# Kernel tuning notes

Measured on AMD Instinct MI355X. Metric: run time of the kernel, lower is better.

The kernel has to match this reference:

```python
import jax, jax.numpy as jnp
import numpy as np

V, D, L, H, FF, B, S = 32000, 2048, 4, 16, 8192, 2, 2048
DH = D // H
PRUNE_LAYERS = (1, 2)   # layers with an attached pruning module
KEEP_RATIO = 0.5        # keep_ratio arg of forward_prefill_with_pruning


def _rms(x, w, eps=1e-6):
    return x * w * jax.lax.rsqrt(jnp.mean(x * x, -1, keepdims=True) + eps)


def _rope(x):
    # x: [B,H,s,DH]; position_ids = arange(s), recomputed after every pruning step
    s = x.shape[2]
    half = DH // 2
    inv = 1.0 / (10000.0 ** (jnp.arange(half, dtype=jnp.float32) / half))
    ang = jnp.arange(s, dtype=jnp.float32)[:, None] * inv  # [s, half]
    cos, sin = jnp.cos(ang), jnp.sin(ang)
    x1, x2 = x[..., :half], x[..., half:]
    return jnp.concatenate([x1 * cos - x2 * sin, x1 * sin + x2 * cos], -1)


def _block(h, mask, wq, wk, wv, wo, wg, wu, wd, ln1, ln2):
    b, s, _ = h.shape
    hn = _rms(h, ln1)
    q = _rope((hn @ wq).reshape(b, s, H, DH).transpose(0, 2, 1, 3))
    k = _rope((hn @ wk).reshape(b, s, H, DH).transpose(0, 2, 1, 3))
    v = (hn @ wv).reshape(b, s, H, DH).transpose(0, 2, 1, 3)
    att = jnp.einsum('bhqd,bhkd->bhqk', q, k) / np.float32(np.sqrt(DH))
    allowed = jnp.tril(jnp.ones((s, s), bool)) & (mask[:, None, None, :] > 0)
    att = jnp.where(allowed, att, jnp.float32(-1e9))
    o = jnp.einsum('bhqk,bhkd->bhqd', jax.nn.softmax(att, -1), v)
    h = h + o.transpose(0, 2, 1, 3).reshape(b, s, D) @ wo
    hn = _rms(h, ln2)
    h = h + (jax.nn.silu(hn @ wg) * (hn @ wu)) @ wd
    return h


def _forward(input_ids, attention_mask, embed, wq, wk, wv, wo, wg, wu, wd, ln1, ln2, lnf, lm_head, scorer):
    h = embed[input_ids]        # [B,S,D]
    mask = attention_mask
    for i in range(L):
        if i in PRUNE_LAYERS:
            pi = PRUNE_LAYERS.index(i)
            # pruning module: Linear(D->2); keep score = logits[..., 0]
            sc = jnp.einsum('bsd,cd->bsc', h, scorer[pi])[..., 0]
            kk = max(1, int(h.shape[1] * KEEP_RATIO))      # static under jit
            _, idx = jax.lax.top_k(sc, kk)
            idx = jnp.sort(idx, -1)                        # sorted kept indices
            h = jnp.take_along_axis(h, idx[..., None], axis=1)
            mask = jnp.take_along_axis(mask, idx, axis=1)
        h = _block(h, mask, wq[i], wk[i], wv[i], wo[i], wg[i], wu[i], wd[i], ln1[i], ln2[i])
    return _rms(h, lnf) @ lm_head   # logits [B, S_pruned, V]


def setup_inputs() -> dict:
    key = jax.random.key(0)
    ks = jax.random.split(key, 12)
    g = lambda k, shape: jax.random.normal(k, shape, jnp.float32) * 0.02
    return {
        'input_ids': jax.random.randint(ks[0], (B, S), 0, V, jnp.int32),
        'attention_mask': jnp.ones((B, S), jnp.int32),
        'embed': g(ks[1], (V, D)),
        'wq': g(ks[2], (L, D, D)),
        'wk': g(ks[3], (L, D, D)),
        'wv': g(ks[4], (L, D, D)),
        'wo': g(ks[5], (L, D, D)),
        'wg': g(ks[6], (L, D, FF)),
        'wu': g(ks[7], (L, D, FF)),
        'wd': g(ks[8], (L, FF, D)),
        'ln1': jnp.ones((L, D), jnp.float32),
        'ln2': jnp.ones((L, D), jnp.float32),
        'lnf': jnp.ones((D,), jnp.float32),
        'lm_head': g(ks[9], (D, V)),
        'scorer': g(ks[10], (len(PRUNE_LAYERS), 2, D)),
    }


def reference(input_ids, attention_mask, embed, wq, wk, wv, wo, wg, wu, wd, ln1, ln2, lnf, lm_head, scorer):
    return _forward(input_ids, attention_mask, embed, wq, wk, wv, wo, wg, wu, wd, ln1, ln2, lnf, lm_head, scorer)
```

## Files before the change

kernel.cpp:

```cpp
#include <hip/hip_runtime.h>
#include <math.h>


#define DD 2048
#define HH 16
#define DHH 128
#define FFF 8192
#define BBATCH 2
#define SSEQ 2048
#define VV 32000
#define LLAYERS 4

typedef float4 f4;
typedef __attribute__((ext_vector_type(8))) short short8;
typedef __attribute__((ext_vector_type(4))) float f32x4;
typedef unsigned short u16;

__device__ inline u16 bf16rne(float x) {
    unsigned u = __float_as_uint(x);
    unsigned r = (u + 0x7FFFu + ((u >> 16) & 1u)) >> 16;
    return (u16)r;
}
__device__ inline float bf16tof(u16 h) {
    return __uint_as_float(((unsigned)h) << 16);
// ... 73 lines not shown
        u16* hp = (u16*)&hv; u16* lp = (u16*)&lv;
#pragma unroll
        for (int j = 0; j < 4; j++) {
            u16 h = bf16rne(o[j]);
            hp[j] = h;
            lp[j] = bf16rne(o[j] - bf16tof(h));
        }
        *(ushort4*)&OH[(size_t)row * DD + i * 4] = hv;
        *(ushort4*)&OL[(size_t)row * DD + i * 4] = lv;
    }
}

__global__ __launch_bounds__(256) void k_cvt_w(const float* __restrict__ W,
                                               u16* __restrict__ WtH,
                                               u16* __restrict__ WtL,
                                               int K, int N, int nc0, int dn0,
                                               int writeLo) {
    __shared__ float T[64][65];
    int tid = threadIdx.x;
    int n0g = nc0 + blockIdx.x * 64;
    int k0  = blockIdx.y * 64;
#pragma unroll
    for (int it = 0; it < 4; it++) {
        int r = it * 16 + (tid >> 4);
        int c4 = (tid & 15) * 4;
        f4 v = *(const f4*)(W + (size_t)(k0 + r) * N + n0g + c4);
        T[r][c4 + 0] = v.x; T[r][c4 + 1] = v.y;
        T[r][c4 + 2] = v.z; T[r][c4 + 3] = v.w;
    }
    __syncthreads();
    int nl = tid >> 2;
    int ks = (tid & 3) * 16;
    u16 hi[16], lo[16];
#pragma unroll
    for (int j = 0; j < 16; j++) {
        float v = T[ks + j][nl];
        u16 h = bf16rne(v);
        hi[j] = h;
        lo[j] = bf16rne(v - bf16tof(h));
    }
    size_t base = (size_t)(dn0 + blockIdx.x * 64 + nl) * K + k0 + ks;
    *(short8*)&WtH[base]     = *(short8*)&hi[0];
    *(short8*)&WtH[base + 8] = *(short8*)&hi[8];
    if (writeLo) {
        *(short8*)&WtL[base]     = *(short8*)&lo[0];
        *(short8*)&WtL[base + 8] = *(short8*)&lo[8];
    }
}

template <int PASSES, int RES, int DUAL>
__global__ __launch_bounds__(256, 2) void k_bgemm(const u16* __restrict__ AH,
                                                  const u16* __restrict__ AL,
                                                  const u16* __restrict__ B1H,
                                                  const u16* __restrict__ B1L,
                                                  const u16* __restrict__ B2H,
                                                  const u16* __restrict__ B2L,
                                                  const float* __restrict__ Rsrc,
                                                  float* __restrict__ C,
                                                  u16* __restrict__ OH,
                                                  u16* __restrict__ OL,
                                                  int M, int ldC, int K) {
    constexpr int NW = DUAL ? 2 : 1;
    __shared__ u16 As[128 * 32];
    __shared__ u16 Bs[NW][128 * 32];
    int tid = threadIdx.x;
    int bx = blockIdx.x, by = blockIdx.y;
    xcd_swz(bx, by);
    int m0 = by * 128, n0 = bx * 128;
    int lane = tid & 63, w = tid >> 6;
    int wm = w >> 1, wn = w & 1;
    int lr = lane & 15, lq = lane >> 4;
    int grow = lane >> 2;
    int gcol = (lane & 3) * 8;

    f32x4 acc[NW][4][4];
#pragma unroll
    for (int u = 0; u < NW; u++)
#pragma unroll
        for (int i = 0; i < 4; i++)
#pragma unroll
            for (int j = 0; j < 4; j++)
#pragma unroll
                for (int r = 0; r < 4; r++) acc[u][i][j][r] = 0.f;

    const int KT = PASSES * K;
    for (int kb = 0; kb < KT; kb += 32) {
        int p  = (PASSES > 1) ? ((kb >= 2 * K) ? 2 : ((kb >= K) ? 1 : 0)) : 0;
        int ks = kb - p * K;
        const u16* Ab = ((p == 2) ? AL  : AH)  + (size_t)(m0 + w * 32) * K + ks;
        const u16* Bb = ((p == 1) ? B1L : B1H) + (size_t)(n0 + w * 32) * K + ks;
        __syncthreads();
        gload16(Ab + (size_t)grow * K + gcol,        &As[w * 1024]);
        gload16(Ab + (size_t)(grow + 16) * K + gcol, &As[w * 1024 + 512]);
        gload16(Bb + (size_t)grow * K + gcol,        &Bs[0][w * 1024]);
        gload16(Bb + (size_t)(grow + 16) * K + gcol, &Bs[0][w * 1024 + 512]);
        if constexpr (DUAL) {
            const u16* B2b = ((p == 1) ? B2L : B2H) + (size_t)(n0 + w * 32) * K + ks;
            gload16(B2b + (size_t)grow * K + gcol,        &Bs[1][w * 1024]);
            gload16(B2b + (size_t)(grow + 16) * K + gcol, &Bs[1][w * 1024 + 512]);
        }
        __syncthreads();
        short8 a[4];
#pragma unroll
        for (int i = 0; i < 4; i++)
            a[i] = *(const short8*)&As[(wm * 64 + i * 16 + lr) * 32 + lq * 8];
#pragma unroll
        for (int u = 0; u < NW; u++) {
#pragma unroll
            for (int j = 0; j < 4; j++) {
                short8 b = *(const short8*)&Bs[u][(wn * 64 + j * 16 + lr) * 32 + lq * 8];
#pragma unroll
                for (int i = 0; i < 4; i++)
                    acc[u][i][j] = __builtin_amdgcn_mfma_f32_16x16x32_bf16(
                        a[i], b, acc[u][i][j], 0, 0, 0);
            }
        }
    }
#pragma unroll
    for (int i = 0; i < 4; i++) {
#pragma unroll
        for (int j = 0; j < 4; j++) {
            int gm = m0 + wm * 64 + i * 16 + lq * 4;
            int gn = n0 + wn * 64 + j * 16 + lr;
#pragma unroll
            for (int r = 0; r < 4; r++) {
                size_t off = (size_t)(gm + r) * ldC + gn;
                if constexpr (DUAL) {
                    float g = acc[0][i][j][r], uu = acc[1][i][j][r];
                    float v = g / (1.0f + expf(-g)) * uu;
                    u16 h = bf16rne(v);
                    OH[off] = h;
                    OL[off] = bf16rne(v - bf16tof(h));
                } else {
                    float v = acc[0][i][j][r];
                    if constexpr (RES) v += Rsrc[off];
                    C[off] = v;
                }
            }
        }
    }
}

template <int PASSES, int PLANE, int EPI>
__global__ __launch_bounds__(512, 2) void k_bg256(const u16* __restrict__ AH,
                                                  const u16* __restrict__ AL,
                                                  const u16* __restrict__ BH,
                                                  const u16* __restrict__ BL,
                                                  float* __restrict__ C,
                                                  u16* __restrict__ OH,
                                                  u16* __restrict__ OL,
                                                  const u16* __restrict__ GEH,
                                                  const u16* __restrict__ GEL,
                                                  int M, int ldC, int K, int ld) {
    __shared__ u16 SM[65536];
    int tid = threadIdx.x;
    int bx = blockIdx.x, by = blockIdx.y;
    xcd_swz(bx, by);
    {
        size_t zo = (size_t)blockIdx.z * K;
        AH += zo; BH += zo;
        if constexpr (PASSES > 1) { AL += zo; BL += zo; }
        if constexpr (!PLANE) C += (size_t)blockIdx.z * ((size_t)M * ldC);
    }
    int m0 = by * 256, n0 = bx * 256;
    int w = tid >> 6, lane = tid & 63;
    int wm = w >> 2, wn = w & 3;
    int lr = lane & 15, lq = lane >> 4;

    f32x4 acc[8][4];
#pragma unroll
    for (int i = 0; i < 8; i++)
#pragma unroll
        for (int j = 0; j < 4; j++)
#pragma unroll
            for (int r = 0; r < 4; r++) acc[i][j][r] = 0.f;

    auto ASRC = [&](int T) -> const u16* {
        int kb = T * 64;
        if (PASSES > 1) {
            if (kb >= 2 * K) return AL + (kb - 2 * K);
            if (kb >= K)     return AH + (kb - K);
        }
        return AH + kb;
    };
    auto BSRC = [&](int T) -> const u16* {
        int kb = T * 64;
        if (PASSES > 1) {
            if (kb >= 2 * K) return BH + (kb - 2 * K);
            if (kb >= K)     return BL + (kb - K);
        }
        return BH + kb;
    };
    int srr = lane >> 3;
    int scc = ((lane & 7) ^ srr) * 8;
    auto STAGE_A = [&](int T, int h, int buf) {
        const u16* s = ASRC(T) + (size_t)(m0 + h * 128 + w * 16 + srr) * ld + scc;
        u16* d = SM + buf * 32768 + h * 8192 + w * 16 * 64;
        gload16(s, d);
        gload16(s + (size_t)8 * ld, d + 8 * 64);
    };
    auto STAGE_B = [&](int T, int h, int buf) {
        const u16* s = BSRC(T) + (size_t)(n0 + h * 128 + w * 16 + srr) * ld + scc;
        u16* d = SM + buf * 32768 + 16384 + h * 8192 + w * 16 * 64;
        gload16(s, d);
        gload16(s + (size_t)8 * ld, d + 8 * 64);
    };
    auto RD_A = [&](const u16* SMb, int MH, short8 (&aF)[4][2]) {
        const u16* Ab = SMb + MH * 8192;
#pragma unroll
        for (int i = 0; i < 4; i++)
#pragma unroll
            for (int kk = 0; kk < 2; kk++)
                aF[i][kk] = *(const short8*)&Ab[(wm * 64 + i * 16 + lr) * 64 +
                                                (((kk * 4 + lq) ^ (lr & 7)) * 8)];
    };
    auto RD_B = [&](const u16* SMb, int NH, short8 (&bF)[2][2]) {
        const u16* Bb = SMb + 16384 + NH * 8192;
#pragma unroll
        for (int j = 0; j < 2; j++)
#pragma unroll
            for (int kk = 0; kk < 2; kk++)
                bF[j][kk] = *(const short8*)&Bb[(wn * 32 + j * 16 + lr) * 64 +
                                                (((kk * 4 + lq) ^ (lr & 7)) * 8)];
    };

    const int NT = (PASSES * K) >> 6;
    STAGE_A(0, 0, 0); STAGE_B(0, 0, 0);
    STAGE_A(0, 1, 0); STAGE_B(0, 1, 0);
    asm volatile("s_waitcnt vmcnt(0)" ::: "memory");
    BARRIER();

    for (int T = 0; T < NT; T++) {
        int cur = T & 1;
        const u16* SMb = SM + cur * 32768;
        short8 a0[4][2], a1[4][2], b0[2][2], b1[2][2];
        if (T + 1 < NT) { STAGE_A(T + 1, 0, cur ^ 1); STAGE_B(T + 1, 0, cur ^ 1); }
        RD_A(SMb, 0, a0);
        RD_B(SMb, 0, b0);
        if (T + 1 < NT) { STAGE_A(T + 1, 1, cur ^ 1); STAGE_B(T + 1, 1, cur ^ 1); }
        RD_B(SMb, 1, b1);
        RD_A(SMb, 1, a1);
        __builtin_amdgcn_s_setprio(1);
#pragma unroll
        for (int kk = 0; kk < 2; kk++)
#pragma unroll
            for (int j = 0; j < 2; j++)
#pragma unroll
                for (int i = 0; i < 4; i++)
                    acc[i][j] = __builtin_amdgcn_mfma_f32_16x16x32_bf16(
                        a0[i][kk], b0[j][kk], acc[i][j], 0, 0, 0);
#pragma unroll
        for (int kk = 0; kk < 2; kk++)
#pragma unroll
            for (int j = 0; j < 2; j++)
#pragma unroll
                for (int i = 0; i < 4; i++)
                    acc[i][2 + j] = __builtin_amdgcn_mfma_f32_16x16x32_bf16(
                        a0[i][kk], b1[j][kk], acc[i][2 + j], 0, 0, 0);
#pragma unroll
        for (int kk = 0; kk < 2; kk++)
#pragma unroll
            for (int j = 0; j < 2; j++)
#pragma unroll
                for (int i = 0; i < 4; i++)
                    acc[4 + i][j] = __builtin_amdgcn_mfma_f32_16x16x32_bf16(
                        a1[i][kk], b0[j][kk], acc[4 + i][j], 0, 0, 0);
#pragma unroll
        for (int kk = 0; kk < 2; kk++)
#pragma unroll
            for (int j = 0; j < 2; j++)
#pragma unroll
                for (int i = 0; i < 4; i++)
                    acc[4 + i][2 + j] = __builtin_amdgcn_mfma_f32_16x16x32_bf16(
                        a1[i][kk], b1[j][kk], acc[4 + i][2 + j], 0, 0, 0);
        __builtin_amdgcn_s_setprio(0);
        if (T + 1 < NT) {
            asm volatile("s_waitcnt vmcnt(0)" ::: "memory");
            BARRIER();
        }
    }

#pragma unroll
    for (int i16 = 0; i16 < 8; i16++) {
#pragma unroll
        for (int jj = 0; jj < 4; jj++) {
            int gm = m0 + (i16 >> 2) * 128 + wm * 64 + (i16 & 3) * 16 + lq * 4;
            int gn = n0 + (jj >> 1) * 128 + wn * 32 + (jj & 1) * 16 + lr;
#pragma unroll
            for (int r = 0; r < 4; r++) {
                size_t off = (size_t)(gm + r) * ldC + gn;
                float v = acc[i16][jj][r];
                if constexpr (PLANE) {
                    if constexpr (EPI) {
                        float g = bf16tof(GEH[off]) + bf16tof(GEL[off]);
                        v = g / (1.0f + expf(-g)) * v;
                    }
                    u16 h = bf16rne(v);
                    OH[off] = h;
                    OL[off] = bf16rne(v - bf16tof(h));
                } else {
                    C[off] = v;
                }
            }
        }
    }
}

__global__ void k_rope_table(float* __restrict__ cosT, float* __restrict__ sinT) {
    int idx = blockIdx.x * blockDim.x + threadIdx.x;
    if (idx >= SSEQ * 64) return;
    int pos = idx >> 6, d = idx & 63;
    float p   = (float)pow(10000.0, (double)d * (1.0 / 64.0));
    float inv = 1.0f / p;
    float ang = (float)pos * inv;
    cosT[idx] = (float)cos((double)ang);
    sinT[idx] = (float)sin((double)ang);
}

__global__ void k_rope(float* __restrict__ C,
                       const float* __restrict__ cosT, const float* __restrict__ sinT,
                       int s, int ld) {
    int bi = blockIdx.x;
    int h = bi % HH;
    int i = (bi / HH) % s;
    size_t base = (size_t)(bi / HH) * ld + h * DHH;
    int d = threadIdx.x;
    float c  = cosT[i * 64 + d];
    float sn = sinT[i * 64 + d];
    float x1 = C[base + d], x2 = C[base + 64 + d];
    C[base + d]      = x1 * c - x2 * sn;
    C[base + 64 + d] = x1 * sn + x2 * c;
    x1 = C[base + 2048 + d]; x2 = C[base + 2048 + 64 + d];
    C[base + 2048 + d]      = x1 * c - x2 * sn;
    C[base + 2048 + 64 + d] = x1 * sn + x2 * c;
}

__global__ __launch_bounds__(256) void k_cvt_qkr(const float* __restrict__ C,
                                                 const float* __restrict__ cosT,
                                                 const float* __restrict__ sinT,
                                                 u16* __restrict__ QHp, u16* __restrict__ QLp,
                                                 u16* __restrict__ KHp, u16* __restrict__ KLp,
                                                 int s) {
    int row = blockIdx.x;
    int i = row % s;
    int c = threadIdx.x * 8;
    int d = c & 127;
    int hi2 = (d >= 64) ? 1 : 0;
    int dd = d - hi2 * 64;
    const float* tb = cosT + (size_t)i * 64;
    const float* ts = sinT + (size_t)i * 64;
#pragma unroll
    for (int sec = 0; sec < 2; sec++) {
        const float* src = C + (size_t)row * 6144 + sec * 2048;
        int base1 = c - hi2 * 64;
        float o[8];
#pragma unroll
        for (int q = 0; q < 2; q++) {
            f4 v1 = *(const f4*)(src + base1 + q * 4);
            f4 v2 = *(const f4*)(src + base1 + 64 + q * 4);
            float a1[4] = {v1.x, v1.y, v1.z, v1.w};
            float a2[4] = {v2.x, v2.y, v2.z, v2.w};
#pragma unroll
            for (int e = 0; e < 4; e++) {
                float cc = tb[dd + q * 4 + e];
                float sn = ts[dd + q * 4 + e];
                o[q * 4 + e] = hi2 ? (a1[e] * sn + a2[e] * cc)
                                   : (a1[e] * cc - a2[e] * sn);
            }
        }
        u16 hbuf[8], lbuf[8];
#pragma unroll
        for (int e = 0; e < 8; e++) {
            u16 h = bf16rne(o[e]);
            hbuf[e] = h;
            lbuf[e] = bf16rne(o[e] - bf16tof(h));
        }
        u16* dh = (sec ? KHp : QHp) + (size_t)row * 2048 + c;
        u16* dl = (sec ? KLp : QLp) + (size_t)row * 2048 + c;
        *(short8*)dh = *(short8*)&hbuf[0];
        *(short8*)dl = *(short8*)&lbuf[0];
    }
}

__global__ __launch_bounds__(256) void k_cvt_vt(const float* __restrict__ C,
                                                u16* __restrict__ VtH,
                                                u16* __restrict__ VtL, int s) {
    __shared__ float T[64][132];
    int bh = blockIdx.y;
    int h = bh & 15, b = bh >> 4;
    int kv0 = blockIdx.x * 64;
    int t = threadIdx.x;
#pragma unroll
    for (int it = 0; it < 8; it++) {
        int kv = it * 8 + (t >> 5);
        int c4 = (t & 31) * 4;
        f4 v = *(const f4*)(C + (size_t)((size_t)b * s + kv0 + kv) * 6144 + 4096 + h * 128 + c4);
        T[kv][c4 + 0] = v.x; T[kv][c4 + 1] = v.y;
        T[kv][c4 + 2] = v.z; T[kv][c4 + 3] = v.w;
    }
    __syncthreads();
    int d = t >> 1, seg = t & 1;
    size_t base = ((size_t)bh * 128 + d) * s + kv0 + seg * 32;
#pragma unroll
    for (int g = 0; g < 4; g++) {
        u16 h8[8], l8[8];
#pragma unroll
        for (int e = 0; e < 8; e++) {
            float v = T[seg * 32 + g * 8 + e][d];
            u16 hh = bf16rne(v);
            h8[e] = hh;
            l8[e] = bf16rne(v - bf16tof(hh));
        }
        int gp = (g ^ ((d >> 1) & 3)) * 8;
        *(short8*)&VtH[base + gp] = *(short8*)&h8[0];
        *(short8*)&VtL[base + gp] = *(short8*)&l8[0];
    }
}

template <int PASSES>
__global__ __launch_bounds__(256, 2) void k_attn_mfma(
        const u16* __restrict__ QHp, const u16* __restrict__ QLp,
        const u16* __restrict__ KHp, const u16* __restrict__ KLp,
        const u16* __restrict__ VtH, const u16* __restrict__ VtL,
        const int* __restrict__ mask,
        u16* __restrict__ OH, u16* __restrict__ OL, int s) {
    constexpr int BUFU = (PASSES > 1) ? 16384 : 8192;
    constexpr int VOFF = (PASSES > 1) ? 8192 : 4096;
    __shared__ u16 SM[2 * BUFU + 5120];
    int tid = threadIdx.x, lane = tid & 63, w = tid >> 6;
    int lr = lane & 15, lq = lane >> 4;
    int grow = lane >> 2;
    int sgcol = (((lane & 3) ^ ((lane >> 3) & 3))) * 8;
    int gcol  = (lane & 3) * 8;
    int rc = (lq ^ ((lr >> 1) & 3)) * 8;
    int gx = gridDim.x;
    int NB = gx * gridDim.y;
    int orig = blockIdx.y * gx + blockIdx.x;
    int qq = NB >> 3, rr = NB & 7;
    int xcd = orig & 7, loc = orig >> 3;
    int swz = (xcd < rr ? xcd * (qq + 1) : rr * (qq + 1) + (xcd - rr) * qq) + loc;
    int bh = swz / gx;
    int qt = gx - 1 - (swz % gx);
    int h = bh & 15, b = bh >> 4;
    int q0 = qt * 128;
// ... 346 lines not shown
                                              int* __restrict__ flg, int s, int kk) {
    int b = blockIdx.x / s, i = blockIdx.x % s;
    const float* scb = sc + (size_t)b * s;
    float vi = scb[i];
    int cnt = 0;
    for (int j = threadIdx.x; j < s; j += 256) {
        float vj = scb[j];
        if (vj > vi || (vj == vi && j < i)) cnt++;
    }
    for (int o = 32; o > 0; o >>= 1) cnt += __shfl_down(cnt, o);
    __shared__ int red[4];
    int wid = threadIdx.x >> 6, lane = threadIdx.x & 63;
    if (lane == 0) red[wid] = cnt;
    __syncthreads();
    if (threadIdx.x == 0) flg[b * s + i] = ((red[0] + red[1] + red[2] + red[3]) < kk) ? 1 : 0;
}

__global__ void k_compact(const int* __restrict__ flg, int* __restrict__ idx, int s, int kk) {
    int b = blockIdx.x;
    if (threadIdx.x == 0) {
        int p = 0;
        for (int i = 0; i < s; i++)
            if (flg[b * s + i]) idx[b * kk + (p++)] = i;
    }
}

__global__ void k_gather(const float* __restrict__ Hin, const int* __restrict__ idx,
                         float* __restrict__ Hout, int s, int kk) {
    int row = blockIdx.x;
    int b = row / kk, p = row % kk;
    int i = idx[b * kk + p];
    const f4* src = (const f4*)(Hin + (size_t)(b * s + i) * DD);
    f4* dst = (f4*)(Hout + (size_t)row * DD);
    for (int t = threadIdx.x; t < DD / 4; t += blockDim.x) dst[t] = src[t];
}

__global__ void k_gather_mask(const int* __restrict__ Min, const int* __restrict__ idx,
                              int* __restrict__ Mout, int s, int kk) {
    int t = blockIdx.x * blockDim.x + threadIdx.x;
    if (t < BBATCH * kk) {
        int b = t / kk, p = t % kk;
        Mout[t] = Min[b * s + idx[b * kk + p]];
    }
}

extern "C" void kernel_launch(void* const* d_in, const int* in_sizes, int n_in,
                              void* d_out, int out_size, void* d_ws, size_t ws_size,
                              hipStream_t stream) {
    const int*   input_ids = (const int*)d_in[0];
    const int*   attn_mask = (const int*)d_in[1];
    const float* embed     = (const float*)d_in[2];
    const float* wq        = (const float*)d_in[3];
    const float* wk        = (const float*)d_in[4];
    const float* wv        = (const float*)d_in[5];
    const float* wo        = (const float*)d_in[6];
    const float* wg        = (const float*)d_in[7];
    const float* wu        = (const float*)d_in[8];
    const float* wd        = (const float*)d_in[9];
    const float* ln1       = (const float*)d_in[10];
    const float* ln2       = (const float*)d_in[11];
    const float* lnf       = (const float*)d_in[12];
    const float* lm_head   = (const float*)d_in[13];
    const float* scorer    = (const float*)d_in[14];

    float* ws = (float*)d_ws;
    const size_t R = (size_t)BBATCH * SSEQ * DD;
    const size_t MISC_FLOATS = 2 * SSEQ * 64 + 5 * (size_t)BBATCH * SSEQ + 1024;
    const size_t NEED_A = (14 * R + MISC_FLOATS) * 4;
    const bool bigws = (ws_size >= NEED_A);

    float* H0   = ws;
    float* H1   = ws + R;
    float* CQKV = ws + 2 * R;
    u16*   AH   = (u16*)(ws + 5 * R);
    u16*   AL   = AH + (size_t)4096 * DD;

    u16* QHp = (u16*)(ws + 6 * R);
    u16* QLp = QHp + (size_t)4096 * DD;
    u16* KHp = (u16*)(ws + 7 * R);
    u16* KLp = KHp + (size_t)4096 * DD;
    u16* VtH = (u16*)(ws + 8 * R);
    u16* VtL = VtH + (size_t)4096 * DD;
    u16* FH  = (u16*)(ws + 6 * R);
    u16* FL  = (u16*)(ws + 8 * R);
    u16* WH1 = (u16*)(ws + 10 * R);
    u16* WL1 = WH1 + (size_t)FFF * DD;
    u16* WH2 = (u16*)(ws + 12 * R);
    u16* WL2 = WH2 + (size_t)FFF * DD;
    u16* WDH = (u16*)(ws + 10 * R);
    u16* WDL = WDH + (size_t)DD * FFF;
    u16* WQKVH = (u16*)(ws + 10 * R);
    u16* WQKVL = WQKVH + (size_t)6144 * DD;

    u16* cWgH = (u16*)CQKV;
    u16* cWgL = cWgH + (size_t)2048 * DD;
    u16* cWuH = cWgL + (size_t)2048 * DD;
    u16* cWuL = cWuH + (size_t)2048 * DD;
    u16* cFH  = (u16*)(ws + 3 * R);
    u16* cFL  = cFH + (size_t)4096 * 2048;
    u16* cWdH = (u16*)(ws + 4 * R);
    u16* cWdL = cWdH + (size_t)2048 * DD;

    float* miscB = ws + (bigws ? 14 * R : 6 * R);
    float* COS = miscB;
    float* SIN = COS + SSEQ * 64;
    float* SC  = SIN + SSEQ * 64;
    int*   FLG = (int*)(SC + (size_t)BBATCH * SSEQ);
    int*   IDX = FLG + BBATCH * SSEQ;
    int*   M0  = IDX + BBATCH * SSEQ;
    int*   M1  = M0 + BBATCH * SSEQ;

    k_rope_table<<<(SSEQ * 64 + 255) / 256, 256, 0, stream>>>(COS, SIN);
    k_embed<<<BBATCH * SSEQ, 256, 0, stream>>>(input_ids, embed, H0);
    k_copy_int<<<(BBATCH * SSEQ + 255) / 256, 256, 0, stream>>>(attn_mask, M0, BBATCH * SSEQ);

    float* Hc = H0; float* Nc = H1;
    int*   Mc = M0; int*   Mt = M1;
    int s = SSEQ;

    for (int l = 0; l < LLAYERS; l++) {
        if (l == 1 || l == 2) {
            int pi = l - 1;
            int kk = s / 2;
            k_score<<<BBATCH * s, 256, 0, stream>>>(Hc, scorer + (size_t)pi * 2 * DD, SC);
            k_rank<<<BBATCH * s, 256, 0, stream>>>(SC, FLG, s, kk);
            k_compact<<<BBATCH, 64, 0, stream>>>(FLG, IDX, s, kk);
            k_gather<<<BBATCH * kk, 256, 0, stream>>>(Hc, IDX, Nc, s, kk);
            k_gather_mask<<<(BBATCH * kk + 255) / 256, 256, 0, stream>>>(Mc, IDX, Mt, s, kk);
            { float* t = Hc; Hc = Nc; Nc = t; }
            { int* t = Mc; Mc = Mt; Mt = t; }
            s = kk;
        }
        int rows = BBATCH * s;
        const bool hiP = (l < 2);
        const int wlo = hiP ? 1 : 0;
        const float* Wq = wq + (size_t)l * DD * DD;
        const float* Wk = wk + (size_t)l * DD * DD;
        const float* Wv = wv + (size_t)l * DD * DD;
        const float* Wo = wo + (size_t)l * DD * DD;
        const float* Wg = wg + (size_t)l * DD * FFF;
        const float* Wu = wu + (size_t)l * DD * FFF;
        const float* Wd = wd + (size_t)l * FFF * DD;
        const float* L1 = ln1 + (size_t)l * DD;
        const float* L2 = ln2 + (size_t)l * DD;

        dim3 gWd(DD / 64, DD / 64);

        k_rmsnorm_cvt<<<rows, 256, 0, stream>>>(Hc, L1, AH, AL);
        if (bigws) {
            k_cvt_w<<<gWd, 256, 0, stream>>>(Wq, WQKVH, WQKVL, DD, DD, 0, 0, wlo);
            k_cvt_w<<<gWd, 256, 0, stream>>>(Wk, WQKVH, WQKVL, DD, DD, 0, 2048, wlo);
            k_cvt_w<<<gWd, 256, 0, stream>>>(Wv, WQKVH, WQKVL, DD, DD, 0, 4096, wlo);
            if (rows >= 2048) {
                dim3 gQKV(6144 / 256, rows / 256);
                if (hiP) k_bg256<3,0,0><<<gQKV,512,0,stream>>>(AH,AL,WQKVH,WQKVL,CQKV,nullptr,nullptr,nullptr,nullptr,rows,6144,DD,DD);
                else     k_bg256<1,0,0><<<gQKV,512,0,stream>>>(AH,AL,WQKVH,WQKVL,CQKV,nullptr,nullptr,nullptr,nullptr,rows,6144,DD,DD);
            } else {
                dim3 gQKV(6144 / 128, rows / 128);
                k_bgemm<1,0,0><<<gQKV,256,0,stream>>>(AH,AL,WQKVH,WQKVL,nullptr,nullptr,nullptr,CQKV,nullptr,nullptr,rows,6144,DD);
            }
        } else {
            u16* WtH = (u16*)Nc;
            u16* WtL = WtH + (size_t)DD * DD;
            dim3 gG(DD / 128, rows / 128);
            const float* Wqkv[3] = {Wq, Wk, Wv};
            for (int q3 = 0; q3 < 3; q3++) {
                k_cvt_w<<<gWd, 256, 0, stream>>>(Wqkv[q3], WtH, WtL, DD, DD, 0, 0, wlo);
                float* Cb = CQKV + q3 * 2048;
                if (hiP) k_bgemm<3,0,0><<<gG,256,0,stream>>>(AH,AL,WtH,WtL,nullptr,nullptr,nullptr,Cb,nullptr,nullptr,rows,6144,DD);
                else     k_bgemm<1,0,0><<<gG,256,0,stream>>>(AH,AL,WtH,WtL,nullptr,nullptr,nullptr,Cb,nullptr,nullptr,rows,6144,DD);
            }
        }

        if (bigws) {
            k_cvt_qkr<<<rows, 256, 0, stream>>>(CQKV, COS, SIN, QHp, QLp, KHp, KLp, s);
            k_cvt_vt<<<dim3(s / 64, BBATCH * HH), 256, 0, stream>>>(CQKV, VtH, VtL, s);
            if (hiP) k_attn_mfma<3><<<dim3(s / 128, BBATCH * HH), 256, 0, stream>>>(
                         QHp, QLp, KHp, KLp, VtH, VtL, Mc, AH, AL, s);
            else     k_attn_mfma<1><<<dim3(s / 128, BBATCH * HH), 256, 0, stream>>>(
                         QHp, QLp, KHp, KLp, VtH, VtL, Mc, AH, AL, s);
        } else {
            k_rope<<<rows * HH, 64, 0, stream>>>(CQKV, COS, SIN, s, 6144);
            k_attn_f32<<<dim3(s / 64, BBATCH * HH), 256, 0, stream>>>(
                CQKV, CQKV + 2048, CQKV + 4096, Mc, AH, AL, s, 6144);
        }

        {
            u16* WtH = bigws ? WQKVH : (u16*)Nc;
            u16* WtL = bigws ? (WQKVH + (size_t)DD * DD) : ((u16*)Nc + (size_t)DD * DD);
            k_cvt_w<<<gWd, 256, 0, stream>>>(Wo, WtH, WtL, DD, DD, 0, 0, wlo);
            if (bigws) {
                int SK = 8192 / rows;
                float* P = ws + 2 * R;
                dim3 g(DD / 256, rows / 256, SK);
                if (hiP) k_bg256<3,0,0><<<g, 512, 0, stream>>>(AH, AL, WtH, WtL, P,
                                nullptr, nullptr, nullptr, nullptr, rows, DD, DD / SK, DD);
                else     k_bg256<1,0,0><<<g, 512, 0, stream>>>(AH, AL, WtH, WtL, P,
                                nullptr, nullptr, nullptr, nullptr, rows, DD, DD / SK, DD);
                long len = (long)rows * DD;
                k_addN<<<(len / 4 + 255) / 256, 256, 0, stream>>>(Hc, P, len, SK);
            } else {
                dim3 gG(DD / 128, rows / 128);
                if (hiP) k_bgemm<3,1,0><<<gG,256,0,stream>>>(AH,AL,WtH,WtL,nullptr,nullptr,Hc,Hc,nullptr,nullptr,rows,DD,DD);
                else     k_bgemm<1,1,0><<<gG,256,0,stream>>>(AH,AL,WtH,WtL,nullptr,nullptr,Hc,Hc,nullptr,nullptr,rows,DD,DD);
            }
        }

        k_rmsnorm_cvt<<<rows, 256, 0, stream>>>(Hc, L2, AH, AL);
        if (bigws && rows >= 2048) {
            k_cvt_w<<<dim3(FFF / 64, DD / 64), 256, 0, stream>>>(Wg, WH1, WL1, DD, FFF, 0, 0, wlo);
            k_cvt_w<<<dim3(FFF / 64, DD / 64), 256, 0, stream>>>(Wu, WH2, WL2, DD, FFF, 0, 0, wlo);
            u16* Gh = (l == 0) ? (u16*)(ws + R) : (u16*)(ws + 2 * R);
            u16* Gl = (u16*)(ws + 3 * R);
            dim3 gMLP(FFF / 256, rows / 256);
            if (hiP) {
                k_bg256<3,1,0><<<gMLP,512,0,stream>>>(AH,AL,WH1,WL1,nullptr,Gh,Gl,nullptr,nullptr,rows,FFF,DD,DD);
                k_bg256<3,1,1><<<gMLP,512,0,stream>>>(AH,AL,WH2,WL2,nullptr,FH,FL,Gh,Gl,rows,FFF,DD,DD);
            } else {
                k_bg256<1,1,0><<<gMLP,512,0,stream>>>(AH,AL,WH1,WL1,nullptr,Gh,Gl,nullptr,nullptr,rows,FFF,DD,DD);
                k_bg256<1,1,1><<<gMLP,512,0,stream>>>(AH,AL,WH2,WL2,nullptr,FH,FL,Gh,Gl,rows,FFF,DD,DD);
            }
            k_cvt_w<<<dim3(DD / 64, FFF / 64), 256, 0, stream>>>(Wd, WDH, WDL, FFF, DD, 0, 0, wlo);
            int SK = 8192 / rows;
            float* P = ws + 2 * R;
            dim3 gD(DD / 256, rows / 256, SK);
            if (hiP) k_bg256<3,0,0><<<gD,512,0,stream>>>(FH,FL,WDH,WDL,P,nullptr,nullptr,nullptr,nullptr,rows,DD,FFF/SK,FFF);
            else     k_bg256<1,0,0><<<gD,512,0,stream>>>(FH,FL,WDH,WDL,P,nullptr,nullptr,nullptr,nullptr,rows,DD,FFF/SK,FFF);
            long len = (long)rows * DD;
            k_addN<<<(len / 4 + 255) / 256, 256, 0, stream>>>(Hc, P, len, SK);
        } else if (bigws) {
            k_cvt_w<<<dim3(FFF / 64, DD / 64), 256, 0, stream>>>(Wg, WH1, WL1, DD, FFF, 0, 0, wlo);
            k_cvt_w<<<dim3(FFF / 64, DD / 64), 256, 0, stream>>>(Wu, WH2, WL2, DD, FFF, 0, 0, wlo);
            k_bgemm<1,0,1><<<dim3(FFF/128, rows/128),256,0,stream>>>(AH,AL,WH1,WL1,WH2,WL2,nullptr,nullptr,FH,FL,rows,FFF,DD);
            k_cvt_w<<<dim3(DD / 64, FFF / 64), 256, 0, stream>>>(Wd, WDH, WDL, FFF, DD, 0, 0, wlo);
            int SK = 8192 / rows;
            float* P = ws + 2 * R;
            dim3 gD(DD / 256, rows / 256, SK);
            k_bg256<1,0,0><<<gD,512,0,stream>>>(FH,FL,WDH,WDL,P,nullptr,nullptr,nullptr,nullptr,rows,DD,FFF/SK,FFF);
            long len = (long)rows * DD;
            k_addN<<<(len / 4 + 255) / 256, 256, 0, stream>>>(Hc, P, len, SK);
        } else {
            for (int ffc = 0; ffc < FFF; ffc += 2048) {
                k_cvt_w<<<dim3(2048 / 64, DD / 64), 256, 0, stream>>>(Wg, cWgH, cWgL, DD, FFF, ffc, 0, wlo);
                k_cvt_w<<<dim3(2048 / 64, DD / 64), 256, 0, stream>>>(Wu, cWuH, cWuL, DD, FFF, ffc, 0, wlo);
                if (hiP) k_bgemm<3,0,1><<<dim3(16, rows/128),256,0,stream>>>(AH,AL,cWgH,cWgL,cWuH,cWuL,nullptr,nullptr,cFH,cFL,rows,2048,DD);
                else     k_bgemm<1,0,1><<<dim3(16, rows/128),256,0,stream>>>(AH,AL,cWgH,cWgL,cWuH,cWuL,nullptr,nullptr,cFH,cFL,rows,2048,DD);
                k_cvt_w<<<dim3(DD / 64, 2048 / 64), 256, 0, stream>>>(Wd + (size_t)ffc * DD, cWdH, cWdL, 2048, DD, 0, 0, wlo);
                if (hiP) k_bgemm<3,1,0><<<dim3(DD/128, rows/128),256,0,stream>>>(cFH,cFL,cWdH,cWdL,nullptr,nullptr,Hc,Hc,nullptr,nullptr,rows,DD,2048);
                else     k_bgemm<1,1,0><<<dim3(DD/128, rows/128),256,0,stream>>>(cFH,cFL,cWdH,cWdL,nullptr,nullptr,Hc,Hc,nullptr,nullptr,rows,DD,2048);
            }
        }
    }

    int rows = BBATCH * s;
    u16* AHf = (u16*)Nc;
    u16* ALf = AHf + (size_t)rows * DD;
    u16* LmH = bigws ? (u16*)(ws + 6 * R) : (u16*)CQKV;
    k_rmsnorm_cvt<<<rows, 256, 0, stream>>>(Hc, lnf, AHf, ALf);
    k_cvt_w<<<dim3(VV / 64, DD / 64), 256, 0, stream>>>(lm_head, LmH, LmH, DD, VV, 0, 0, 0);
    if (bigws) {
        k_bg256<1,0,0><<<dim3(VV / 256, rows / 256), 512, 0, stream>>>(
            AHf, ALf, LmH, LmH, (float*)d_out, nullptr, nullptr, nullptr, nullptr,
            rows, VV, DD, DD);
    } else {
        k_bgemm<1,0,0><<<dim3(VV / 128, rows / 128), 256, 0, stream>>>(
            AHf, ALf, LmH, LmH, nullptr, nullptr, nullptr, (float*)d_out,
            nullptr, nullptr, rows, VV, DD);
    }
}
```

Baseline: 4.322 ms.

## Shrink big GEMM tile to 128x256 with triple-buffered two-ahead prefetch

The 512-thread bf16 GEMM kernel now computes 128x256 output tiles instead of 256x256. It uses three LDS stages and prefetches two K-steps ahead, waiting with a partial vmcnt rather than draining all loads each iteration. Every launch site doubles its M grid dimension to match. The aim is to hide global-load latency and put more blocks on the CUs for the pruned row counts, at the cost of lower reuse per tile and more LDS per block.

```diff
diff --git a/kernel.cpp b/kernel.cpp
--- a/kernel.cpp
+++ b/kernel.cpp
@@ -249,7 +249,7 @@
                                                   const u16* __restrict__ GEH,
                                                   const u16* __restrict__ GEL,
                                                   int M, int ldC, int K, int ld) {
-    __shared__ u16 SM[65536];
+    __shared__ u16 SM[73728];
     int tid = threadIdx.x;
     int bx = blockIdx.x, by = blockIdx.y;
     xcd_swz(bx, by);
@@ -259,14 +259,14 @@
         if constexpr (PASSES > 1) { AL += zo; BL += zo; }
         if constexpr (!PLANE) C += (size_t)blockIdx.z * ((size_t)M * ldC);
     }
-    int m0 = by * 256, n0 = bx * 256;
+    int m0 = by * 128, n0 = bx * 256;
     int w = tid >> 6, lane = tid & 63;
     int wm = w >> 2, wn = w & 3;
     int lr = lane & 15, lq = lane >> 4;
 
-    f32x4 acc[8][4];
-#pragma unroll
-    for (int i = 0; i < 8; i++)
+    f32x4 acc[4][4];
+#pragma unroll
+    for (int i = 0; i < 4; i++)
 #pragma unroll
         for (int j = 0; j < 4; j++)
 #pragma unroll
@@ -290,103 +290,75 @@
     };
     int srr = lane >> 3;
     int scc = ((lane & 7) ^ srr) * 8;
-    auto STAGE_A = [&](int T, int h, int buf) {
-        const u16* s = ASRC(T) + (size_t)(m0 + h * 128 + w * 16 + srr) * ld + scc;
-        u16* d = SM + buf * 32768 + h * 8192 + w * 16 * 64;
-        gload16(s, d);
-        gload16(s + (size_t)8 * ld, d + 8 * 64);
+    auto STAGE = [&](int T, int buf) {
+        u16* bb = SM + buf * 24576;
+        const u16* sa = ASRC(T) + (size_t)(m0 + w * 16 + srr) * ld + scc;
+        u16* da = bb + (w * 16) * 64;
+        gload16(sa, da);
+        gload16(sa + (size_t)8 * ld, da + 8 * 64);
+        const u16* sb0 = BSRC(T) + (size_t)(n0 + w * 16 + srr) * ld + scc;
+        u16* db0 = bb + 8192 + (w * 16) * 64;
+        gload16(sb0, db0);
+        gload16(sb0 + (size_t)8 * ld, db0 + 8 * 64);
+        const u16* sb1 = BSRC(T) + (size_t)(n0 + 128 + w * 16 + srr) * ld + scc;
+        u16* db1 = bb + 16384 + (w * 16) * 64;
+        gload16(sb1, db1);
+        gload16(sb1 + (size_t)8 * ld, db1 + 8 * 64);
     };
-    auto STAGE_B = [&](int T, int h, int buf) {
-        const u16* s = BSRC(T) + (size_t)(n0 + h * 128 + w * 16 + srr) * ld + scc;
-        u16* d = SM + buf * 32768 + 16384 + h * 8192 + w * 16 * 64;
-        gload16(s, d);
-        gload16(s + (size_t)8 * ld, d + 8 * 64);
-    };
-    auto RD_A = [&](const u16* SMb, int MH, short8 (&aF)[4][2]) {
-        const u16* Ab = SMb + MH * 8192;
+
+    const int NT = (PASSES * K) >> 6;
+    STAGE(0, 0);
+    STAGE(1, 1);
+    asm volatile("s_waitcnt vmcnt(6)" ::: "memory");
+    BARRIER();
+
+    int cur = 0;
+    for (int T = 0; T < NT; T++) {
+        int nxt2 = cur + 2; if (nxt2 >= 3) nxt2 -= 3;
+        if (T + 2 < NT) STAGE(T + 2, nxt2);
+        const u16* Ab = SM + cur * 24576;
+        const u16* Bb = Ab + 8192;
+        short8 aF[4][2], bF[4][2];
 #pragma unroll
         for (int i = 0; i < 4; i++)
 #pragma unroll
             for (int kk = 0; kk < 2; kk++)
                 aF[i][kk] = *(const short8*)&Ab[(wm * 64 + i * 16 + lr) * 64 +
                                                 (((kk * 4 + lq) ^ (lr & 7)) * 8)];
-    };
-    auto RD_B = [&](const u16* SMb, int NH, short8 (&bF)[2][2]) {
-        const u16* Bb = SMb + 16384 + NH * 8192;
-#pragma unroll
-        for (int j = 0; j < 2; j++)
+#pragma unroll
+        for (int j = 0; j < 4; j++)
 #pragma unroll
             for (int kk = 0; kk < 2; kk++)
-                bF[j][kk] = *(const short8*)&Bb[(wn * 32 + j * 16 + lr) * 64 +
+                bF[j][kk] = *(const short8*)&Bb[(wn * 64 + j * 16 + lr) * 64 +
                                                 (((kk * 4 + lq) ^ (lr & 7)) * 8)];
-    };
-
-    const int NT = (PASSES * K) >> 6;
-    STAGE_A(0, 0, 0); STAGE_B(0, 0, 0);
-    STAGE_A(0, 1, 0); STAGE_B(0, 1, 0);
-    asm volatile("s_waitcnt vmcnt(0)" ::: "memory");
-    BARRIER();
-
-    for (int T = 0; T < NT; T++) {
-        int cur = T & 1;
-        const u16* SMb = SM + cur * 32768;
-        short8 a0[4][2], a1[4][2], b0[2][2], b1[2][2];
-        if (T + 1 < NT) { STAGE_A(T + 1, 0, cur ^ 1); STAGE_B(T + 1, 0, cur ^ 1); }
-        RD_A(SMb, 0, a0);
-        RD_B(SMb, 0, b0);
-        if (T + 1 < NT) { STAGE_A(T + 1, 1, cur ^ 1); STAGE_B(T + 1, 1, cur ^ 1); }
-        RD_B(SMb, 1, b1);
-        RD_A(SMb, 1, a1);
         __builtin_amdgcn_s_setprio(1);
 #pragma unroll
         for (int kk = 0; kk < 2; kk++)
 #pragma unroll
-            for (int j = 0; j < 2; j++)
+            for (int j = 0; j < 4; j++)
 #pragma unroll
                 for (int i = 0; i < 4; i++)
                     acc[i][j] = __builtin_amdgcn_mfma_f32_16x16x32_bf16(
-                        a0[i][kk], b0[j][kk], acc[i][j], 0, 0, 0);
-#pragma unroll
-        for (int kk = 0; kk < 2; kk++)
-#pragma unroll
-            for (int j = 0; j < 2; j++)
-#pragma unroll
-                for (int i = 0; i < 4; i++)
-                    acc[i][2 + j] = __builtin_amdgcn_mfma_f32_16x16x32_bf16(
-                        a0[i][kk], b1[j][kk], acc[i][2 + j], 0, 0, 0);
-#pragma unroll
-        for (int kk = 0; kk < 2; kk++)
-#pragma unroll
-            for (int j = 0; j < 2; j++)
-#pragma unroll
-                for (int i = 0; i < 4; i++)
-                    acc[4 + i][j] = __builtin_amdgcn_mfma_f32_16x16x32_bf16(
-                        a1[i][kk], b0[j][kk], acc[4 + i][j], 0, 0, 0);
-#pragma unroll
-        for (int kk = 0; kk < 2; kk++)
-#pragma unroll
-            for (int j = 0; j < 2; j++)
-#pragma unroll
-                for (int i = 0; i < 4; i++)
-                    acc[4 + i][2 + j] = __builtin_amdgcn_mfma_f32_16x16x32_bf16(
-                        a1[i][kk], b1[j][kk], acc[4 + i][2 + j], 0, 0, 0);
+                        aF[i][kk], bF[j][kk], acc[i][j], 0, 0, 0);
         __builtin_amdgcn_s_setprio(0);
         if (T + 1 < NT) {
-            asm volatile("s_waitcnt vmcnt(0)" ::: "memory");
+            if (T + 2 < NT) asm volatile("s_waitcnt vmcnt(6)" ::: "memory");
+            else            asm volatile("s_waitcnt vmcnt(0)" ::: "memory");
             BARRIER();
         }
-    }
-
-#pragma unroll
-    for (int i16 = 0; i16 < 8; i16++) {
-#pragma unroll
-        for (int jj = 0; jj < 4; jj++) {
-            int gm = m0 + (i16 >> 2) * 128 + wm * 64 + (i16 & 3) * 16 + lq * 4;
-            int gn = n0 + (jj >> 1) * 128 + wn * 32 + (jj & 1) * 16 + lr;
+        cur = (cur + 1 == 3) ? 0 : cur + 1;
+    }
+
+#pragma unroll
+    for (int i = 0; i < 4; i++) {
+#pragma unroll
+        for (int j = 0; j < 4; j++) {
+            int gm = m0 + wm * 64 + i * 16 + lq * 4;
+            int gn = n0 + wn * 64 + j * 16 + lr;
 #pragma unroll
             for (int r = 0; r < 4; r++) {
                 size_t off = (size_t)(gm + r) * ldC + gn;
-                float v = acc[i16][jj][r];
+                float v = acc[i][j][r];
                 if constexpr (PLANE) {
                     if constexpr (EPI) {
                         float g = bf16tof(GEH[off]) + bf16tof(GEL[off]);
@@ -1039,7 +1011,7 @@
             k_cvt_w<<<gWd, 256, 0, stream>>>(Wk, WQKVH, WQKVL, DD, DD, 0, 2048, wlo);
             k_cvt_w<<<gWd, 256, 0, stream>>>(Wv, WQKVH, WQKVL, DD, DD, 0, 4096, wlo);
             if (rows >= 2048) {
-                dim3 gQKV(6144 / 256, rows / 256);
+                dim3 gQKV(6144 / 256, rows / 128);
                 if (hiP) k_bg256<3,0,0><<<gQKV,512,0,stream>>>(AH,AL,WQKVH,WQKVL,CQKV,nullptr,nullptr,nullptr,nullptr,rows,6144,DD,DD);
                 else     k_bg256<1,0,0><<<gQKV,512,0,stream>>>(AH,AL,WQKVH,WQKVL,CQKV,nullptr,nullptr,nullptr,nullptr,rows,6144,DD,DD);
             } else {
@@ -1079,7 +1051,7 @@
             if (bigws) {
                 int SK = 8192 / rows;
                 float* P = ws + 2 * R;
-                dim3 g(DD / 256, rows / 256, SK);
+                dim3 g(DD / 256, rows / 128, SK);
                 if (hiP) k_bg256<3,0,0><<<g, 512, 0, stream>>>(AH, AL, WtH, WtL, P,
                                 nullptr, nullptr, nullptr, nullptr, rows, DD, DD / SK, DD);
                 else     k_bg256<1,0,0><<<g, 512, 0, stream>>>(AH, AL, WtH, WtL, P,
@@ -1099,7 +1071,7 @@
             k_cvt_w<<<dim3(FFF / 64, DD / 64), 256, 0, stream>>>(Wu, WH2, WL2, DD, FFF, 0, 0, wlo);
             u16* Gh = (l == 0) ? (u16*)(ws + R) : (u16*)(ws + 2 * R);
             u16* Gl = (u16*)(ws + 3 * R);
-            dim3 gMLP(FFF / 256, rows / 256);
+            dim3 gMLP(FFF / 256, rows / 128);
             if (hiP) {
                 k_bg256<3,1,0><<<gMLP,512,0,stream>>>(AH,AL,WH1,WL1,nullptr,Gh,Gl,nullptr,nullptr,rows,FFF,DD,DD);
                 k_bg256<3,1,1><<<gMLP,512,0,stream>>>(AH,AL,WH2,WL2,nullptr,FH,FL,Gh,Gl,rows,FFF,DD,DD);
@@ -1110,7 +1082,7 @@
             k_cvt_w<<<dim3(DD / 64, FFF / 64), 256, 0, stream>>>(Wd, WDH, WDL, FFF, DD, 0, 0, wlo);
             int SK = 8192 / rows;
             float* P = ws + 2 * R;
-            dim3 gD(DD / 256, rows / 256, SK);
+            dim3 gD(DD / 256, rows / 128, SK);
             if (hiP) k_bg256<3,0,0><<<gD,512,0,stream>>>(FH,FL,WDH,WDL,P,nullptr,nullptr,nullptr,nullptr,rows,DD,FFF/SK,FFF);
             else     k_bg256<1,0,0><<<gD,512,0,stream>>>(FH,FL,WDH,WDL,P,nullptr,nullptr,nullptr,nullptr,rows,DD,FFF/SK,FFF);
             long len = (long)rows * DD;
@@ -1122,7 +1094,7 @@
             k_cvt_w<<<dim3(DD / 64, FFF / 64), 256, 0, stream>>>(Wd, WDH, WDL, FFF, DD, 0, 0, wlo);
             int SK = 8192 / rows;
             float* P = ws + 2 * R;
-            dim3 gD(DD / 256, rows / 256, SK);
+            dim3 gD(DD / 256, rows / 128, SK);
             k_bg256<1,0,0><<<gD,512,0,stream>>>(FH,FL,WDH,WDL,P,nullptr,nullptr,nullptr,nullptr,rows,DD,FFF/SK,FFF);
             long len = (long)rows * DD;
             k_addN<<<(len / 4 + 255) / 256, 256, 0, stream>>>(Hc, P, len, SK);
@@ -1146,7 +1118,7 @@
     k_rmsnorm_cvt<<<rows, 256, 0, stream>>>(Hc, lnf, AHf, ALf);
     k_cvt_w<<<dim3(VV / 64, DD / 64), 256, 0, stream>>>(lm_head, LmH, LmH, DD, VV, 0, 0, 0);
     if (bigws) {
-        k_bg256<1,0,0><<<dim3(VV / 256, rows / 256), 512, 0, stream>>>(
+        k_bg256<1,0,0><<<dim3(VV / 256, rows / 128), 512, 0, stream>>>(
             AHf, ALf, LmH, LmH, (float*)d_out, nullptr, nullptr, nullptr, nullptr,
             rows, VV, DD, DD);
     } else {
```

Result: slower. 4.998 ms (+15.6%).
